# Kernel tuning notes

Measured on AMD Instinct MI355X. Metric: run time of the kernel, lower is better.

The kernel has to match this reference:

```python
import jax, jax.numpy as jnp
import numpy as np


def setup_inputs() -> dict:
    key = jax.random.key(0)
    M, N = 2048, 16384
    x = jax.random.normal(key, (M, N), dtype=jnp.float32)
    # expk per DREAMPlace get_expk: exp(-j*pi*n/(2N)) stored as [N, 2] = (cos, -sin)
    ang = jnp.arange(N, dtype=jnp.float32) * np.float32(np.pi / (2.0 * N))
    expk = jnp.stack([jnp.cos(ang), -jnp.sin(ang)], axis=-1)
    return {"x": x, "expk": expk}


def reference(x, expk):
    """IDXCT: y_k = Re{ sum_{n=0}^{N-1} x_n * exp(j*pi/(2N) * n * (2k+1)) }.

    O(N log N) via the FFT trick:
      y_k = Re{ sum_n [x_n * exp(j*pi*n/(2N))] * exp(j*2*pi*n*k/(2N)) }
          = 2N * Re{ IFFT_{2N}(zero-padded v)[k] },  v_n = x_n * conj(expk_n)
    """
    N = x.shape[-1]
    # expk encodes exp(-j*pi*n/(2N)); we need its conjugate exp(+j*pi*n/(2N))
    v = x * (expk[..., 0] - 1j * expk[..., 1])  # complex64, [M, N]
    V = jnp.fft.ifft(v, n=2 * N, axis=-1)       # zero-padded to 2N
    y = (2 * N) * jnp.real(V[..., :N])
    return y.astype(x.dtype)
```

## Files before the change

### kernel.cpp

```cpp
#include <hip/hip_runtime.h>

#define PI_F 3.14159265358979323846f

constexpr int N_COLS   = 16384;
constexpr int HALF     = 8192;
constexpr int NTHREADS = 1024;

__device__ __forceinline__ int sw(int a) {
    return a ^ ((a >> 5) & 31) ^ ((a >> 10) & 31);
}

__global__ __launch_bounds__(NTHREADS)
void idxct_kernel(const float* __restrict__ x,
                  const float* __restrict__ expk,
                  float* __restrict__ y)
{
    __shared__ float sre[HALF];
    __shared__ float sim[HALF];

    const int row = blockIdx.x;
    const float* __restrict__ xr = x + (size_t)row * N_COLS;
    float* __restrict__ yr       = y + (size_t)row * N_COLS;
    const int t = threadIdx.x;
    const float x0 = xr[0];
    const float2* __restrict__ ek2 = (const float2*)expk;

    #pragma unroll
    for (int i = 0; i < HALF / NTHREADS; ++i) {
        int k = t + i * NTHREADS;
        float vkr, vki, c0, s0;
        {
            float2 e = ek2[k];
            c0 = e.x; s0 = -e.y;
            if (k == 0) { vkr = x0; vki = 0.0f; }
            else {
                float a = xr[k], b = xr[N_COLS - k];
                vkr = a * c0 + b * s0;
                vki = a * s0 - b * c0;
            }
        }
        float wkr, wki;
        {
            int K = k + HALF;
            float2 e = ek2[K];
            float c = e.x, s = -e.y;
            float a = xr[K], b = xr[N_COLS - K];
            wkr = a * c + b * s;
            wki = a * s - b * c;
        }
        float dr = vkr - wkr, di = vki - wki;
        float cA = c0 * c0 - s0 * s0, sA = 2.0f * c0 * s0;
        float ec = cA * cA - sA * sA, es = 2.0f * cA * sA;
        float zr = (vkr + wkr) - (ec * di + es * dr);
        float zi = (vki + wki) + (ec * dr - es * di);
        int rk = (int)(__brev((unsigned)k) >> 19);
        int pa = sw(rk);
        sre[pa] = zr;
        sim[pa] = zi;
    }

    __syncthreads();
    #pragma unroll
    for (int u = 0; u < 2; ++u) {
        int q = t + u * NTHREADS;
        int a0 = sw(q << 2);
        int a1 = a0 ^ 1, a2i = a0 ^ 2, a3 = a0 ^ 3;
        float r0 = sre[a0],  i0 = sim[a0];
        float r1 = sre[a1],  i1 = sim[a1];
        float r2 = sre[a2i], i2 = sim[a2i];
        float r3 = sre[a3],  i3 = sim[a3];
        float tr, ti;
        tr = r1;  ti = i1;  r1 = r0 - tr; i1 = i0 - ti; r0 += tr; i0 += ti;
        tr = r3;  ti = i3;  r3 = r2 - tr; i3 = i2 - ti; r2 += tr; i2 += ti;
        tr = r2;  ti = i2;  r2 = r0 - tr; i2 = i0 - ti; r0 += tr; i0 += ti;
        tr = -i3; ti = r3;  r3 = r1 - tr; i3 = i1 - ti; r1 += tr; i1 += ti;
        sre[a0]  = r0; sim[a0]  = i0;
        sre[a1]  = r1; sim[a1]  = i1;
        sre[a2i] = r2; sim[a2i] = i2;
        sre[a3]  = r3; sim[a3]  = i3;
    }

    #pragma unroll
    for (int p = 1; p < 6; ++p) {
        const int s = 1 << (2 * p);
        __syncthreads();
        #pragma unroll
        for (int u = 0; u < 2; ++u) {
            int q = t + u * NTHREADS;
            int j = q & (s - 1);
            int base = ((q >> (2 * p)) << (2 * p + 2)) + j;
            int a0 = sw(base);
            int a1 = sw(base + s);
            int a2i = sw(base + 2 * s);
            int a3 = sw(base + 3 * s);
            float r0 = sre[a0],  i0 = sim[a0];
            float r1 = sre[a1],  i1 = sim[a1];
            float r2 = sre[a2i], i2 = sim[a2i];
            float r3 = sre[a3],  i3 = sim[a3];
            float a2ang = (float)j * (PI_F / (float)(2 * s));
            float s2, c2; __sincosf(a2ang, &s2, &c2);
            float c1 = c2 * c2 - s2 * s2;
            float s1 = 2.0f * c2 * s2;
            float tr, ti;
            tr = c1 * r1 - s1 * i1; ti = c1 * i1 + s1 * r1;
            r1 = r0 - tr; i1 = i0 - ti; r0 += tr; i0 += ti;
            tr = c1 * r3 - s1 * i3; ti = c1 * i3 + s1 * r3;
            r3 = r2 - tr; i3 = i2 - ti; r2 += tr; i2 += ti;
            tr = c2 * r2 - s2 * i2; ti = c2 * i2 + s2 * r2;
            r2 = r0 - tr; i2 = i0 - ti; r0 += tr; i0 += ti;
            tr = -s2 * r3 - c2 * i3; ti = c2 * r3 - s2 * i3;
            r3 = r1 - tr; i3 = i1 - ti; r1 += tr; i1 += ti;
            sre[a0]  = r0; sim[a0]  = i0;
            sre[a1]  = r1; sim[a1]  = i1;
            sre[a2i] = r2; sim[a2i] = i2;
            sre[a3]  = r3; sim[a3]  = i3;
        }
    }

    __syncthreads();
    #pragma unroll
    for (int u = 0; u < 4; ++u) {
        int q = t + u * NTHREADS;
        float a = (float)q * (PI_F / 4096.0f);
        float sn, cs; __sincosf(a, &sn, &cs);
        int a0 = sw(q);
        int a1 = sw(q + 4096);
        float r0 = sre[a0], i0 = sim[a0];
        float r1 = sre[a1], i1 = sim[a1];
        float tr = cs * r1 - sn * i1;
        float ti = cs * i1 + sn * r1;
        sre[a0] = r0 + tr; sim[a0] = i0 + ti;
        sre[a1] = r0 - tr; sim[a1] = i0 - ti;
    }
    __syncthreads();

    #pragma unroll
    for (int i = 0; i < N_COLS / NTHREADS; ++i) {
        int q = t + i * NTHREADS;
        int pidx = (q & 1) ? (N_COLS - 1 - (q >> 1)) : (q >> 1);
        int zi = sw(pidx >> 1);
        float val = (pidx & 1) ? sim[zi] : sre[zi];
        yr[q] = 0.5f * (val + x0);
    }
}

extern "C" void kernel_launch(void* const* d_in, const int* in_sizes, int n_in,
                              void* d_out, int out_size, void* d_ws, size_t ws_size,
                              hipStream_t stream)
{
    const float* x    = (const float*)d_in[0];
    const float* expk = (const float*)d_in[1];
    float* y          = (float*)d_out;
    const int M = in_sizes[0] / N_COLS;
    idxct_kernel<<<dim3(M), dim3(NTHREADS), 0, stream>>>(x, expk, y);
}
```

Baseline: 259.9 us.

## Restructure shared-memory FFT into radix-16 rounds with table twiddles and vector stores

Rewrites the per-row FFT so each thread does radix-16 passes held in registers (three rounds plus a final radix-2) instead of six radix-4 passes. This cuts shared-memory round trips and barriers. Twiddles now come from the expk table rather than __sincosf. Shared storage changes from split re/im arrays to interleaved float2 with a new swizzle, and the output is written as float4 stores. The block shrinks to 512 threads with launch bounds for 4 blocks per CU, which raises register pressure per thread in exchange for fewer LDS passes.

```diff
diff --git a/kernel.cpp b/kernel.cpp
--- a/kernel.cpp
+++ b/kernel.cpp
@@ -1,146 +1,147 @@
 #include <hip/hip_runtime.h>
 
-#define PI_F 3.14159265358979323846f
+constexpr int N_COLS = 16384;
+constexpr int HALF   = 8192;
+constexpr int NT     = 512;
 
-constexpr int N_COLS   = 16384;
-constexpr int HALF     = 8192;
-constexpr int NTHREADS = 1024;
-
-__device__ __forceinline__ int sw(int a) {
-    return a ^ ((a >> 5) & 31) ^ ((a >> 10) & 31);
+__host__ __device__ constexpr int Sc(int p) {
+    return p ^ ((p >> 4) & 15) ^ ((p >> 8) & 31);
+}
+__host__ __device__ constexpr int br4(int c) {
+    return ((c & 1) << 3) | ((c & 2) << 1) | ((c & 4) >> 1) | ((c & 8) >> 3);
 }
 
-__global__ __launch_bounds__(NTHREADS)
+__device__ __forceinline__ void bf4(float& r0, float& i0, float& r1, float& i1,
+                                    float& r2, float& i2, float& r3, float& i3,
+                                    float cw, float sw) {
+    float c1 = cw * cw - sw * sw;
+    float s1 = 2.0f * cw * sw;
+    float tr, ti;
+    tr = c1 * r1 - s1 * i1; ti = c1 * i1 + s1 * r1;
+    r1 = r0 - tr; i1 = i0 - ti; r0 += tr; i0 += ti;
+    tr = c1 * r3 - s1 * i3; ti = c1 * i3 + s1 * r3;
+    r3 = r2 - tr; i3 = i2 - ti; r2 += tr; i2 += ti;
+    tr = cw * r2 - sw * i2; ti = cw * i2 + sw * r2;
+    r2 = r0 - tr; i2 = i0 - ti; r0 += tr; i0 += ti;
+    tr = -sw * r3 - cw * i3; ti = cw * r3 - sw * i3;
+    r3 = r1 - tr; i3 = i1 - ti; r1 += tr; i1 += ti;
+}
+
+template<int SS>
+__device__ __forceinline__ void round16(float2* zs, const float2* __restrict__ ek2,
+                                        int sb, int j) {
+    float vr[4][4], vi[4][4];
+    #pragma unroll
+    for (int c2 = 0; c2 < 4; ++c2)
+        #pragma unroll
+        for (int c1 = 0; c1 < 4; ++c1) {
+            float2 v = zs[sb ^ Sc(SS * c1 + 4 * SS * c2)];
+            vr[c2][c1] = v.x; vi[c2][c1] = v.y;
+        }
+    {
+        float2 e = ek2[j * (16384 / SS)];
+        float cw = e.x, sw = -e.y;
+        #pragma unroll
+        for (int c2 = 0; c2 < 4; ++c2)
+            bf4(vr[c2][0], vi[c2][0], vr[c2][1], vi[c2][1],
+                vr[c2][2], vi[c2][2], vr[c2][3], vi[c2][3], cw, sw);
+    }
+    #pragma unroll
+    for (int c1 = 0; c1 < 4; ++c1) {
+        float2 e = ek2[j * (4096 / SS) + c1 * 4096];
+        bf4(vr[0][c1], vi[0][c1], vr[1][c1], vi[1][c1],
+            vr[2][c1], vi[2][c1], vr[3][c1], vi[3][c1], e.x, -e.y);
+    }
+    #pragma unroll
+    for (int c2 = 0; c2 < 4; ++c2)
+        #pragma unroll
+        for (int c1 = 0; c1 < 4; ++c1)
+            zs[sb ^ Sc(SS * c1 + 4 * SS * c2)] = make_float2(vr[c2][c1], vi[c2][c1]);
+}
+
+__global__ __launch_bounds__(NT, 4)
 void idxct_kernel(const float* __restrict__ x,
                   const float* __restrict__ expk,
                   float* __restrict__ y)
 {
-    __shared__ float sre[HALF];
-    __shared__ float sim[HALF];
+    __shared__ float2 zs[HALF];
 
     const int row = blockIdx.x;
     const float* __restrict__ xr = x + (size_t)row * N_COLS;
     float* __restrict__ yr       = y + (size_t)row * N_COLS;
-    const int t = threadIdx.x;
+    const int t   = threadIdx.x;
     const float x0 = xr[0];
     const float2* __restrict__ ek2 = (const float2*)expk;
 
+    const int spt = Sc((int)(__brev((unsigned)t) >> 19));
     #pragma unroll
-    for (int i = 0; i < HALF / NTHREADS; ++i) {
-        int k = t + i * NTHREADS;
-        float vkr, vki, c0, s0;
-        {
-            float2 e = ek2[k];
-            c0 = e.x; s0 = -e.y;
-            if (k == 0) { vkr = x0; vki = 0.0f; }
-            else {
-                float a = xr[k], b = xr[N_COLS - k];
-                vkr = a * c0 + b * s0;
-                vki = a * s0 - b * c0;
-            }
+    for (int c = 0; c < 16; ++c) {
+        const int k = t + NT * c;
+        float2 e0 = ek2[k];
+        float c0 = e0.x, s0 = -e0.y;
+        float vkr, vki;
+        if (c == 0 && t == 0) { vkr = x0; vki = 0.0f; }
+        else {
+            float a = xr[k], b = xr[N_COLS - k];
+            vkr = a * c0 + b * s0;
+            vki = a * s0 - b * c0;
         }
-        float wkr, wki;
-        {
-            int K = k + HALF;
-            float2 e = ek2[K];
-            float c = e.x, s = -e.y;
-            float a = xr[K], b = xr[N_COLS - K];
-            wkr = a * c + b * s;
-            wki = a * s - b * c;
-        }
+        const int K = k + HALF;
+        float2 e1 = ek2[K];
+        float c4 = e1.x, s4 = -e1.y;
+        float a1 = xr[K], b1 = xr[N_COLS - K];
+        float wkr = a1 * c4 + b1 * s4;
+        float wki = a1 * s4 - b1 * c4;
         float dr = vkr - wkr, di = vki - wki;
         float cA = c0 * c0 - s0 * s0, sA = 2.0f * c0 * s0;
         float ec = cA * cA - sA * sA, es = 2.0f * cA * sA;
         float zr = (vkr + wkr) - (ec * di + es * dr);
         float zi = (vki + wki) + (ec * dr - es * di);
-        int rk = (int)(__brev((unsigned)k) >> 19);
-        int pa = sw(rk);
-        sre[pa] = zr;
-        sim[pa] = zi;
+        zs[spt ^ br4(c)] = make_float2(zr, zi);
     }
 
     __syncthreads();
-    #pragma unroll
-    for (int u = 0; u < 2; ++u) {
-        int q = t + u * NTHREADS;
-        int a0 = sw(q << 2);
-        int a1 = a0 ^ 1, a2i = a0 ^ 2, a3 = a0 ^ 3;
-        float r0 = sre[a0],  i0 = sim[a0];
-        float r1 = sre[a1],  i1 = sim[a1];
-        float r2 = sre[a2i], i2 = sim[a2i];
-        float r3 = sre[a3],  i3 = sim[a3];
-        float tr, ti;
-        tr = r1;  ti = i1;  r1 = r0 - tr; i1 = i0 - ti; r0 += tr; i0 += ti;
-        tr = r3;  ti = i3;  r3 = r2 - tr; i3 = i2 - ti; r2 += tr; i2 += ti;
-        tr = r2;  ti = i2;  r2 = r0 - tr; i2 = i0 - ti; r0 += tr; i0 += ti;
-        tr = -i3; ti = r3;  r3 = r1 - tr; i3 = i1 - ti; r1 += tr; i1 += ti;
-        sre[a0]  = r0; sim[a0]  = i0;
-        sre[a1]  = r1; sim[a1]  = i1;
-        sre[a2i] = r2; sim[a2i] = i2;
-        sre[a3]  = r3; sim[a3]  = i3;
-    }
+    round16<1>(zs, ek2, Sc(t << 4), 0);
+    __syncthreads();
+    round16<16>(zs, ek2, Sc(((t >> 4) << 8) | (t & 15)), t & 15);
+    __syncthreads();
+    round16<256>(zs, ek2, Sc(((t >> 8) << 12) | (t & 255)), t & 255);
+    __syncthreads();
 
-    #pragma unroll
-    for (int p = 1; p < 6; ++p) {
-        const int s = 1 << (2 * p);
-        __syncthreads();
+    {
+        const int st = Sc(t);
         #pragma unroll
-        for (int u = 0; u < 2; ++u) {
-            int q = t + u * NTHREADS;
-            int j = q & (s - 1);
-            int base = ((q >> (2 * p)) << (2 * p + 2)) + j;
-            int a0 = sw(base);
-            int a1 = sw(base + s);
-            int a2i = sw(base + 2 * s);
-            int a3 = sw(base + 3 * s);
-            float r0 = sre[a0],  i0 = sim[a0];
-            float r1 = sre[a1],  i1 = sim[a1];
-            float r2 = sre[a2i], i2 = sim[a2i];
-            float r3 = sre[a3],  i3 = sim[a3];
-            float a2ang = (float)j * (PI_F / (float)(2 * s));
-            float s2, c2; __sincosf(a2ang, &s2, &c2);
-            float c1 = c2 * c2 - s2 * s2;
-            float s1 = 2.0f * c2 * s2;
-            float tr, ti;
-            tr = c1 * r1 - s1 * i1; ti = c1 * i1 + s1 * r1;
-            r1 = r0 - tr; i1 = i0 - ti; r0 += tr; i0 += ti;
-            tr = c1 * r3 - s1 * i3; ti = c1 * i3 + s1 * r3;
-            r3 = r2 - tr; i3 = i2 - ti; r2 += tr; i2 += ti;
-            tr = c2 * r2 - s2 * i2; ti = c2 * i2 + s2 * r2;
-            r2 = r0 - tr; i2 = i0 - ti; r0 += tr; i0 += ti;
-            tr = -s2 * r3 - c2 * i3; ti = c2 * r3 - s2 * i3;
-            r3 = r1 - tr; i3 = i1 - ti; r1 += tr; i1 += ti;
-            sre[a0]  = r0; sim[a0]  = i0;
-            sre[a1]  = r1; sim[a1]  = i1;
-            sre[a2i] = r2; sim[a2i] = i2;
-            sre[a3]  = r3; sim[a3]  = i3;
+        for (int c = 0; c < 8; ++c) {
+            const int q   = t + NT * c;
+            const int sq  = st ^ Sc(NT * c);
+            const int sq2 = sq ^ Sc(4096);
+            float2 a = zs[sq], b = zs[sq2];
+            float cw, sw;
+            if (c < 4) { float2 e = ek2[q << 3];          cw = e.x; sw = -e.y; }
+            else       { float2 e = ek2[(q - 2048) << 3]; cw = e.y; sw =  e.x; }
+            float tr = cw * b.x - sw * b.y;
+            float ti = cw * b.y + sw * b.x;
+            zs[sq]  = make_float2(a.x + tr, a.y + ti);
+            zs[sq2] = make_float2(a.x - tr, a.y - ti);
         }
-    }
-
-    __syncthreads();
-    #pragma unroll
-    for (int u = 0; u < 4; ++u) {
-        int q = t + u * NTHREADS;
-        float a = (float)q * (PI_F / 4096.0f);
-        float sn, cs; __sincosf(a, &sn, &cs);
-        int a0 = sw(q);
-        int a1 = sw(q + 4096);
-        float r0 = sre[a0], i0 = sim[a0];
-        float r1 = sre[a1], i1 = sim[a1];
-        float tr = cs * r1 - sn * i1;
-        float ti = cs * i1 + sn * r1;
-        sre[a0] = r0 + tr; sim[a0] = i0 + ti;
-        sre[a1] = r0 - tr; sim[a1] = i0 - ti;
     }
     __syncthreads();
 
-    #pragma unroll
-    for (int i = 0; i < N_COLS / NTHREADS; ++i) {
-        int q = t + i * NTHREADS;
-        int pidx = (q & 1) ? (N_COLS - 1 - (q >> 1)) : (q >> 1);
-        int zi = sw(pidx >> 1);
-        float val = (pidx & 1) ? sim[zi] : sre[zi];
-        yr[q] = 0.5f * (val + x0);
+    {
+        const int st  = Sc(t);
+        const int stc = Sc(t ^ 511);
+        #pragma unroll
+        for (int i = 0; i < 8; ++i) {
+            const int m = t + NT * i;
+            float2 a = zs[st  ^ Sc(NT * i)];
+            float2 b = zs[stc ^ Sc((15 - i) << 9)];
+            float4 o;
+            o.x = 0.5f * (a.x + x0);
+            o.y = 0.5f * (b.y + x0);
+            o.z = 0.5f * (a.y + x0);
+            o.w = 0.5f * (b.x + x0);
+            *reinterpret_cast<float4*>(yr + 4 * m) = o;
+        }
     }
 }
 
@@ -152,5 +153,5 @@
     const float* expk = (const float*)d_in[1];
     float* y          = (float*)d_out;
     const int M = in_sizes[0] / N_COLS;
-    idxct_kernel<<<dim3(M), dim3(NTHREADS), 0, stream>>>(x, expk, y);
+    idxct_kernel<<<dim3(M), dim3(NT), 0, stream>>>(x, expk, y);
 }
```

After: 282.3 us. +8.6%, slower.
